# Kernel optimization log

Hardware: AMD Instinct MI355X
Metric: run time of the kernel (lower is better)

## Reference

```python
import jax, jax.numpy as jnp
import numpy as np
import math

WH, WW = 7, 7          # window size
N = WH * WW            # tokens per window = 49
H = 12                 # num heads
C = 384                # dim
D = C // H             # head dim = 32
NW = 64                # num windows (56x56 map, 7x7 windows)
B = 32                 # image batch
BW = B * NW            # windowed batch = 2048


def _cpb_constants():
    # log-spaced continuous relative coords table, flattened to [(2*WH-1)*(2*WW-1), 2]
    rh = np.arange(-(WH - 1), WH, dtype=np.float32)
    rw = np.arange(-(WW - 1), WW, dtype=np.float32)
    t = np.stack(np.meshgrid(rh, rw, indexing='ij'), axis=-1)  # [13,13,2]
    t[..., 0] /= (WH - 1)
    t[..., 1] /= (WW - 1)
    t *= 8.0
    t = np.sign(t) * np.log2(np.abs(t) + 1.0) / np.log2(8.0)
    # relative position index [N*N]
    ch, cw = np.meshgrid(np.arange(WH), np.arange(WW), indexing='ij')
    cf = np.stack([ch.ravel(), cw.ravel()])            # [2, N]
    rel = cf[:, :, None] - cf[:, None, :]              # [2, N, N]
    rel = rel.transpose(1, 2, 0).astype(np.int64)      # [N, N, 2]
    rel[..., 0] += WH - 1
    rel[..., 1] += WW - 1
    rel[..., 0] *= 2 * WW - 1
    rpi = rel.sum(-1).reshape(-1)                      # [N*N]
    return jnp.asarray(t.reshape(-1, 2)), jnp.asarray(rpi)

_COORDS_TABLE, _RPI = _cpb_constants()


def setup_inputs() -> dict:
    key = jax.random.key(0)
    ks = jax.random.split(key, 8)
    x = jax.random.normal(ks[0], (BW, N, C), dtype=jnp.float32)
    # shifted-window style 0/-100 mask
    mask = jnp.where(jax.random.uniform(ks[1], (NW, N, N)) < 0.1, -100.0, 0.0).astype(jnp.float32)
    qkv_w = jax.random.normal(ks[2], (3 * C, C), dtype=jnp.float32) * 0.02
    q_bias = jnp.zeros((C,), dtype=jnp.float32)
    v_bias = jnp.zeros((C,), dtype=jnp.float32)
    logit_scale = jnp.full((H, 1, 1), math.log(10.0), dtype=jnp.float32)
    cpb_w1 = jax.random.normal(ks[3], (512, 2), dtype=jnp.float32) * 0.02
    cpb_b1 = jnp.zeros((512,), dtype=jnp.float32)
    cpb_w2 = jax.random.normal(ks[4], (H, 512), dtype=jnp.float32) * 0.02
    proj_w = jax.random.normal(ks[5], (C, C), dtype=jnp.float32) * 0.02
    proj_b = jnp.zeros((C,), dtype=jnp.float32)
    return {"x": x, "mask": mask, "qkv_w": qkv_w, "q_bias": q_bias, "v_bias": v_bias,
            "logit_scale": logit_scale, "cpb_w1": cpb_w1, "cpb_b1": cpb_b1,
            "cpb_w2": cpb_w2, "proj_w": proj_w, "proj_b": proj_b}


def reference(x, mask, qkv_w, q_bias, v_bias, logit_scale, cpb_w1, cpb_b1, cpb_w2, proj_w, proj_b):
    B_, n, c = x.shape
    # qkv projection; k has no bias (registered zeros buffer)
    qkv_bias = jnp.concatenate([q_bias, jnp.zeros_like(q_bias), v_bias])
    qkv = x @ qkv_w.T + qkv_bias                              # [B_, N, 3C]
    qkv = qkv.reshape(B_, n, 3, H, D).transpose(2, 0, 3, 1, 4)  # [3, B_, H, N, D]
    q, k, v = qkv[0], qkv[1], qkv[2]
    # cosine attention
    qn = q / jnp.clip(jnp.linalg.norm(q, axis=-1, keepdims=True), 1e-12)
    kn = k / jnp.clip(jnp.linalg.norm(k, axis=-1, keepdims=True), 1e-12)
    attn = jnp.einsum('bhnd,bhmd->bhnm', qn, kn)              # [B_, H, N, N]
    scale = jnp.exp(jnp.minimum(logit_scale, math.log(1.0 / 0.01)))  # [H,1,1]
    attn = attn * scale
    # continuous position bias MLP + gather
    hid = jax.nn.relu(_COORDS_TABLE @ cpb_w1.T + cpb_b1)      # [169, 512]
    bias_tab = hid @ cpb_w2.T                                  # [169, H]
    rpb = bias_tab[_RPI].reshape(n, n, H).transpose(2, 0, 1)  # [H, N, N]
    rpb = 16.0 * jax.nn.sigmoid(rpb)
    attn = attn + rpb[None]
    # shifted-window mask add
    nW = mask.shape[0]
    attn = attn.reshape(B_ // nW, nW, H, n, n) + mask[None, :, None]
    attn = jax.nn.softmax(attn.reshape(B_, H, n, n), axis=-1)
    out = jnp.einsum('bhnm,bhmd->bnhd', attn, v).reshape(B_, n, c)
    return out @ proj_w.T + proj_b
```

## Files before the change

kernel.cpp:

```cpp
#include <hip/hip_runtime.h>
#include <hip/hip_bf16.h>
#include <math.h>

#define NTOK 49
#define NH 12
#define HD 32
#define CDIM 384
#define NWIN 64
#define BWIN 2048
#define QKVROW 1152

typedef __bf16 bf16x8 __attribute__((ext_vector_type(8)));
typedef __bf16 bf16x4 __attribute__((ext_vector_type(4)));
typedef float f32x4 __attribute__((ext_vector_type(4)));

__device__ __forceinline__ void gload_lds16(const void* g, void* l) {
    __builtin_amdgcn_global_load_lds((const __attribute__((address_space(1))) void*)g,
                                     (__attribute__((address_space(3))) void*)l, 16, 0, 0);
}

__global__ void cvt_f32_bf16(const float* __restrict__ src, __bf16* __restrict__ dst, int n8) {
    int i = blockIdx.x * blockDim.x + threadIdx.x;
    if (i >= n8) return;
    f32x4 a = *(const f32x4*)(src + (size_t)i * 8);
    f32x4 b = *(const f32x4*)(src + (size_t)i * 8 + 4);
    bf16x8 o;
#pragma unroll
    for (int e = 0; e < 4; ++e) { o[e] = (__bf16)a[e]; o[e + 4] = (__bf16)b[e]; }
    *(bf16x8*)(dst + (size_t)i * 8) = o;
}

__global__ void cpb_mlp_kernel(const float* __restrict__ w1, const float* __restrict__ b1,
                               const float* __restrict__ w2, float* __restrict__ bias_tab) {
    int t = blockIdx.x * blockDim.x + threadIdx.x;
    if (t >= 169 * NH) return;
    int r = t / NH, h = t - (t / NH) * NH;
    int i = r / 13, j = r - (r / 13) * 13;
    float a0 = (float)(i - 6) * (8.0f / 6.0f);
    float a1 = (float)(j - 6) * (8.0f / 6.0f);
    float c0 = copysignf(log2f(fabsf(a0) + 1.0f) * (1.0f / 3.0f), a0);
    float c1 = copysignf(log2f(fabsf(a1) + 1.0f) * (1.0f / 3.0f), a1);
    float sum = 0.f;
    for (int k = 0; k < 512; ++k) {
        float hid = c0 * w1[2 * k] + c1 * w1[2 * k + 1] + b1[k];
        hid = fmaxf(hid, 0.f);
        sum += hid * w2[h * 512 + k];
    }
    bias_tab[r * NH + h] = sum;
}

__global__ void rpbT_kernel(const float* __restrict__ bias_tab, float* __restrict__ rpbT) {
    int idx = blockIdx.x * blockDim.x + threadIdx.x;
    if (idx >= NH * NTOK * NTOK) return;
    int h = idx / (NTOK * NTOK);
    int rem = idx - h * (NTOK * NTOK);
    int kj = rem / NTOK, qi = rem - (rem / NTOK) * NTOK;
    int chi = qi / 7, cwi = qi - chi * 7;
    int chj = kj / 7, cwj = kj - chj * 7;
    int rpi = (chi - chj + 6) * 13 + (cwi - cwj + 6);
    float x = bias_tab[rpi * NH + h];
    rpbT[idx] = 16.f / (1.f + __expf(-x));
}

__global__ void maskT_kernel(const float* __restrict__ mask, float* __restrict__ maskT) {
    int idx = blockIdx.x * blockDim.x + threadIdx.x;
    if (idx >= NWIN * NTOK * NTOK) return;
    int w = idx / (NTOK * NTOK);
    int rem = idx - w * (NTOK * NTOK);
    int kj = rem / NTOK, qi = rem - (rem / NTOK) * NTOK;
    maskT[idx] = mask[(w * NTOK + qi) * NTOK + kj];
}

template <int MODE, int NBY>
__global__ __launch_bounds__(256) void gemm6(
    const __bf16* __restrict__ A, const __bf16* __restrict__ Bw,
    const float* __restrict__ qbias, const float* __restrict__ vbias,
    __bf16* __restrict__ qkvout,
    float* __restrict__ fout, const float* __restrict__ fbias)
{
    __shared__ __bf16 As[3][128 * 32];
    __shared__ __bf16 Bs[3][128 * 32];
    const int tid = threadIdx.x;
    const int chunk = (784 * NBY) >> 3;
    const int wg = (blockIdx.x & 7) * chunk + (blockIdx.x >> 3);
    const int gx = wg / NBY, gy = wg - (wg / NBY) * NBY;
    const int lane = tid & 63;
    const int wid = tid >> 6;
    const int wr = (wid >> 1) * 64;
    const int wc = (wid & 1) * 64;
    const int fr = lane & 15;
    const int fq = lane >> 4;

    f32x4 acc[4][4];
#pragma unroll
    for (int m = 0; m < 4; ++m)
#pragma unroll
        for (int n = 0; n < 4; ++n)
            acc[m][n] = (f32x4){0.f, 0.f, 0.f, 0.f};

    const int srow0 = tid >> 2, scp0 = tid & 3;
    const int srow1 = (256 + tid) >> 2;
    const size_t ar0 = (size_t)(gx * 128 + srow0) * CDIM + (scp0 ^ ((srow0 >> 1) & 3)) * 8;
    const size_t ar1 = (size_t)(gx * 128 + srow1) * CDIM + (scp0 ^ ((srow1 >> 1) & 3)) * 8;
    const size_t br0 = (size_t)(gy * 128 + srow0) * CDIM + (scp0 ^ ((srow0 >> 1) & 3)) * 8;
    const size_t br1 = (size_t)(gy * 128 + srow1) * CDIM + (scp0 ^ ((srow1 >> 1) & 3)) * 8;
    const int ls0 = tid * 16, ls1 = (256 + tid) * 16;

#define STAGE(ti, buf) do {                                              \
        const int kk_ = (ti) * 32;                                       \
        gload_lds16(A + ar0 + kk_, (char*)&As[buf][0] + ls0);            \
        gload_lds16(A + ar1 + kk_, (char*)&As[buf][0] + ls1);            \
        gload_lds16(Bw + br0 + kk_, (char*)&Bs[buf][0] + ls0);           \
        gload_lds16(Bw + br1 + kk_, (char*)&Bs[buf][0] + ls1);           \
    } while (0)

    STAGE(0, 0);
    STAGE(1, 1);

#pragma unroll
    for (int t = 0; t < 12; ++t) {
        if (t < 11) asm volatile("s_waitcnt vmcnt(4)" ::: "memory");
        else        asm volatile("s_waitcnt vmcnt(0)" ::: "memory");
        __builtin_amdgcn_s_barrier();
        if (t + 2 < 12) STAGE(t + 2, (t + 2) % 3);
        const int cur = t % 3;
        bf16x8 af[4], bfr[4];
#pragma unroll
        for (int m = 0; m < 4; ++m) {
            const int row = wr + m * 16 + fr;
            af[m] = *(const bf16x8*)&As[cur][row * 32 + (fq ^ ((row >> 1) & 3)) * 8];
        }
#pragma unroll
        for (int n = 0; n < 4; ++n) {
            const int row = wc + n * 16 + fr;
            bfr[n] = *(const bf16x8*)&Bs[cur][row * 32 + (fq ^ ((row >> 1) & 3)) * 8];
        }
#pragma unroll
        for (int m = 0; m < 4; ++m)
#pragma unroll
            for (int n = 0; n < 4; ++n)
                acc[m][n] = __builtin_amdgcn_mfma_f32_16x16x32_bf16(af[m], bfr[n], acc[m][n], 0, 0, 0);
    }
#undef STAGE

    if (MODE == 0) {
        const int colbase = gy * 128;
        const int part = colbase / CDIM;
        const int pcolbase = colbase - part * CDIM;
#pragma unroll
        for (int m = 0; m < 4; ++m) {
#pragma unroll
            for (int r = 0; r < 4; ++r) {
                const int row = gx * 128 + wr + m * 16 + fq * 4 + r;
                __bf16* orow = qkvout + (size_t)row * QKVROW + colbase + wc;
#pragma unroll
                for (int n = 0; n < 4; ++n) {
                    const int pcol = pcolbase + wc + n * 16 + fr;
                    float val = acc[m][n][r];
                    if (part == 0) val += qbias[pcol];
                    if (part == 2) val += vbias[pcol];
                    orow[n * 16 + fr] = (__bf16)val;
                }
            }
        }
    } else {
#pragma unroll
        for (int m = 0; m < 4; ++m) {
#pragma unroll
            for (int r = 0; r < 4; ++r) {
                const int row = gx * 128 + wr + m * 16 + fq * 4 + r;
                float* orow = fout + (size_t)row * CDIM + gy * 128 + wc;
#pragma unroll
                for (int n = 0; n < 4; ++n) {
                    const int col = gy * 128 + wc + n * 16 + fr;
                    orow[n * 16 + fr] = acc[m][n][r] + fbias[col];
                }
            }
        }
    }
}

#define WREG 15872
__global__ __launch_bounds__(256) void attn2(
    const __bf16* __restrict__ qkv, const float* __restrict__ maskT,
    const float* __restrict__ rpbT, const float* __restrict__ lscale,
    __bf16* __restrict__ aout)
{
    __shared__ char smem[4 * WREG];
    const int tid = threadIdx.x;
    const int wid = tid >> 6, lane = tid & 63;
    const int bh = blockIdx.x * 4 + wid;
    const int b = bh / NH, h = bh - b * NH;
    const int w = b & (NWIN - 1);
    const int c = lane & 15, g = lane >> 4;

    char* base = smem + wid * WREG;
    __bf16* Kl = (__bf16*)base;
    __bf16* Ql = (__bf16*)(base + 5120);
    __bf16* Vl = (__bf16*)(base + 10240);
    float* invq = (float*)(base + 15360);
    float* invk = (float*)(base + 15616);
    char* Pl = base;

    const float sc = __expf(fminf(lscale[h], 4.6051702f));

    {
        const int row = lane;
        const size_t rb = ((size_t)b * NTOK + row) * QKVROW + h * HD;
        bf16x8 z;
#pragma unroll
        for (int e = 0; e < 8; ++e) z[e] = (__bf16)0.f;
        {
            bf16x8 t[4];
            float ss = 0.f;
            if (row < NTOK) {
#pragma unroll
                for (int ch = 0; ch < 4; ++ch) {
                    t[ch] = *(const bf16x8*)(qkv + rb + ch * 8);
#pragma unroll
                    for (int e = 0; e < 8; ++e) { float f = (float)t[ch][e]; ss += f * f; }
                }
            } else {
#pragma unroll
                for (int ch = 0; ch < 4; ++ch) t[ch] = z;
            }
#pragma unroll
            for (int ch = 0; ch < 4; ++ch) *(bf16x8*)&Ql[row * 40 + ch * 8] = t[ch];
            invq[row] = sc / fmaxf(sqrtf(ss), 1e-12f);
        }
        {
            bf16x8 t[4];
            float ss = 0.f;
            if (row < NTOK) {
#pragma unroll
                for (int ch = 0; ch < 4; ++ch) {
                    t[ch] = *(const bf16x8*)(qkv + rb + CDIM + ch * 8);
#pragma unroll
                    for (int e = 0; e < 8; ++e) { float f = (float)t[ch][e]; ss += f * f; }
                }
            } else {
#pragma unroll
                for (int ch = 0; ch < 4; ++ch) t[ch] = z;
            }
#pragma unroll
            for (int ch = 0; ch < 4; ++ch) *(bf16x8*)&Kl[row * 40 + ch * 8] = t[ch];
            invk[row] = 1.f / fmaxf(sqrtf(ss), 1e-12f);
        }
        {
            bf16x8 t[4];
            if (row < NTOK) {
#pragma unroll
                for (int ch = 0; ch < 4; ++ch) t[ch] = *(const bf16x8*)(qkv + rb + 2 * CDIM + ch * 8);
            } else {
#pragma unroll
                for (int ch = 0; ch < 4; ++ch) t[ch] = z;
            }
#pragma unroll
            for (int ch = 0; ch < 4; ++ch) *(bf16x8*)&Vl[row * 40 + ch * 8] = t[ch];
        }
    }

    bf16x8 kfr[4], qfr[4];
#pragma unroll
    for (int mt = 0; mt < 4; ++mt) kfr[mt] = *(const bf16x8*)&Kl[(mt * 16 + c) * 40 + g * 8];
#pragma unroll
    for (int nt = 0; nt < 4; ++nt) qfr[nt] = *(const bf16x8*)&Ql[(nt * 16 + c) * 40 + g * 8];
    f32x4 S[4][4];
#pragma unroll
    for (int mt = 0; mt < 4; ++mt)
#pragma unroll
        for (int nt = 0; nt < 4; ++nt) {
            S[mt][nt] = (f32x4){0.f, 0.f, 0.f, 0.f};
            S[mt][nt] = __builtin_amdgcn_mfma_f32_16x16x32_bf16(kfr[mt], qfr[nt], S[mt][nt], 0, 0, 0);
        }

    const float* rp = rpbT + h * (NTOK * NTOK);
    const float* mk = maskT + w * (NTOK * NTOK);
    float ivq[4];
#pragma unroll
    for (int nt = 0; nt < 4; ++nt) ivq[nt] = invq[nt * 16 + c];
#pragma unroll
    for (int mt = 0; mt < 4; ++mt) {
#pragma unroll
        for (int r = 0; r < 4; ++r) {
            const int k = mt * 16 + g * 4 + r;
            const float ivk = invk[k];
#pragma unroll
            for (int nt = 0; nt < 4; ++nt) {
                const int q = nt * 16 + c;
                float v = S[mt][nt][r] * ivk * ivq[nt];
                if (k < NTOK) {
                    if (q < NTOK) v += rp[k * NTOK + q] + mk[k * NTOK + q];
                } else {
                    v = -1e30f;
                }
                S[mt][nt][r] = v;
            }
        }
    }

    float rs[4];
#pragma unroll
    for (int nt = 0; nt < 4; ++nt) {
        float m = -1e30f;
#pragma unroll
        for (int mt = 0; mt < 4; ++mt)
#pragma unroll
            for (int r = 0; r < 4; ++r) m = fmaxf(m, S[mt][nt][r]);
        m = fmaxf(m, __shfl_xor(m, 16));
        m = fmaxf(m, __shfl_xor(m, 32));
        float s = 0.f;
#pragma unroll
        for (int mt = 0; mt < 4; ++mt)
#pragma unroll
            for (int r = 0; r < 4; ++r) {
                float e = __expf(S[mt][nt][r] - m);
                S[mt][nt][r] = e;
                s += e;
            }
        s += __shfl_xor(s, 16);
        s += __shfl_xor(s, 32);
        rs[nt] = 1.f / s;
    }

#pragma unroll
    for (int mt = 0; mt < 4; ++mt)
#pragma unroll
        for (int nt = 0; nt < 4; ++nt) {
            bf16x4 pk;
#pragma unroll
            for (int r = 0; r < 4; ++r) pk[r] = (__bf16)(S[mt][nt][r] * rs[nt]);
            *(bf16x4*)(Pl + (nt * 16 + c) * 144 + (mt * 16 + g * 4) * 2) = pk;
        }

    bf16x8 vfr[2][2];
#pragma unroll
    for (int kt = 0; kt < 2; ++kt)
#pragma unroll
        for (int dt = 0; dt < 2; ++dt) {
            bf16x8 t;
#pragma unroll
            for (int e = 0; e < 8; ++e) t[e] = Vl[(kt * 32 + g * 8 + e) * 40 + dt * 16 + c];
            vfr[kt][dt] = t;
        }
    f32x4 O[4][2];
#pragma unroll
    for (int mt = 0; mt < 4; ++mt)
#pragma unroll
        for (int dt = 0; dt < 2; ++dt) O[mt][dt] = (f32x4){0.f, 0.f, 0.f, 0.f};
#pragma unroll
    for (int mt = 0; mt < 4; ++mt)
#pragma unroll
        for (int kt = 0; kt < 2; ++kt) {
            bf16x8 pfr = *(const bf16x8*)(Pl + (mt * 16 + c) * 144 + kt * 64 + g * 16);
#pragma unroll
            for (int dt = 0; dt < 2; ++dt)
                O[mt][dt] = __builtin_amdgcn_mfma_f32_16x16x32_bf16(pfr, vfr[kt][dt], O[mt][dt], 0, 0, 0);
        }

#pragma unroll
    for (int mt = 0; mt < 4; ++mt)
#pragma unroll
        for (int r = 0; r < 4; ++r) {
            const int q = mt * 16 + g * 4 + r;
            if (q < NTOK) {
                const size_t off = ((size_t)b * NTOK + q) * CDIM + h * HD;
                aout[off + c] = (__bf16)O[mt][0][r];
                aout[off + 16 + c] = (__bf16)O[mt][1][r];
            }
        }
}

extern "C" void kernel_launch(void* const* d_in, const int* in_sizes, int n_in,
                              void* d_out, int out_size, void* d_ws, size_t ws_size,
                              hipStream_t stream) {
    const float* x      = (const float*)d_in[0];
    const float* mask   = (const float*)d_in[1];
    const float* qkv_w  = (const float*)d_in[2];
    const float* q_bias = (const float*)d_in[3];
    const float* v_bias = (const float*)d_in[4];
    const float* lscale = (const float*)d_in[5];
    const float* cpb_w1 = (const float*)d_in[6];
    const float* cpb_b1 = (const float*)d_in[7];
    const float* cpb_w2 = (const float*)d_in[8];
    const float* proj_w = (const float*)d_in[9];
    const float* proj_b = (const float*)d_in[10];
    float* out = (float*)d_out;

    const size_t NROWS = (size_t)BWIN * NTOK;
    __bf16* qkvbuf  = (__bf16*)d_ws;
    __bf16* xbf     = qkvbuf + NROWS * QKVROW;
    __bf16* aoutbuf = xbf;
    __bf16* qkv_wb  = xbf + NROWS * CDIM;
    __bf16* proj_wb = qkv_wb + QKVROW * CDIM;
    float*  bias_tab = (float*)(proj_wb + CDIM * CDIM);
    float*  rpbT   = bias_tab + 169 * NH;
    float*  maskT  = rpbT + NH * NTOK * NTOK;

    hipLaunchKernelGGL(cvt_f32_bf16, dim3((int)((NROWS * CDIM / 8 + 255) / 256)), dim3(256), 0, stream,
                       x, xbf, (int)(NROWS * CDIM / 8));
    hipLaunchKernelGGL(cvt_f32_bf16, dim3((QKVROW * CDIM / 8 + 255) / 256), dim3(256), 0, stream,
                       qkv_w, qkv_wb, QKVROW * CDIM / 8);
    hipLaunchKernelGGL(cvt_f32_bf16, dim3((CDIM * CDIM / 8 + 255) / 256), dim3(256), 0, stream,
                       proj_w, proj_wb, CDIM * CDIM / 8);
    hipLaunchKernelGGL(cpb_mlp_kernel, dim3(8), dim3(256), 0, stream,
                       cpb_w1, cpb_b1, cpb_w2, bias_tab);
    hipLaunchKernelGGL(rpbT_kernel, dim3((NH * NTOK * NTOK + 255) / 256), dim3(256), 0, stream,
                       bias_tab, rpbT);
    hipLaunchKernelGGL(maskT_kernel, dim3((NWIN * NTOK * NTOK + 255) / 256), dim3(256), 0, stream,
                       mask, maskT);
    hipLaunchKernelGGL((gemm6<0, 9>), dim3(784 * 9), dim3(256), 0, stream,
                       xbf, qkv_wb, q_bias, v_bias, qkvbuf, (float*)nullptr,
                       (const float*)nullptr);
    hipLaunchKernelGGL(attn2, dim3(BWIN * NH / 4), dim3(256), 0, stream,
                       qkvbuf, maskT, rpbT, lscale, aoutbuf);
    hipLaunchKernelGGL((gemm6<1, 3>), dim3(784 * 3), dim3(256), 0, stream,
                       aoutbuf, proj_wb, (const float*)nullptr, (const float*)nullptr,
                       (__bf16*)nullptr, out, proj_b);
}
```

Baseline: 451.8 us.

## Fuse x fp32-to-bf16 conversion into QKV GEMM and coalesce attention loads

The QKV GEMM now loads fp32 x tiles directly into LDS through global_load_lds and converts them to bf16 when reading fragments. This removes the separate conversion kernel and its full write and re-read of a bf16 copy of x. The cost is double the LDS footprint for the A tile and extra global reads of fp32 data inside the GEMM, and the GEMM is re-run for each of the 9 column tiles. The attention kernel now gives each block 4 consecutive heads of one window and loads Q/K/V cooperatively into LDS with coalesced 16-byte loads, then computes the norms from LDS after a barrier.

```diff
diff --git a/kernel.cpp b/kernel.cpp
--- a/kernel.cpp
+++ b/kernel.cpp
@@ -71,19 +71,125 @@
     maskT[idx] = mask[(w * NTOK + qi) * NTOK + kj];
 }
 
-template <int MODE, int NBY>
-__global__ __launch_bounds__(256) void gemm6(
+__global__ __launch_bounds__(256) void gemm_qkv2(
+    const float* __restrict__ X, const __bf16* __restrict__ Bw,
+    const float* __restrict__ qbias, const float* __restrict__ vbias,
+    __bf16* __restrict__ qkvout)
+{
+    __shared__ float Asf[3][128 * 32];
+    __shared__ __bf16 Bs[3][128 * 32];
+    const int tid = threadIdx.x;
+    const int chunkg = (784 * 9) >> 3;
+    const int wg = (blockIdx.x & 7) * chunkg + (blockIdx.x >> 3);
+    const int gx = wg / 9, gy = wg - (wg / 9) * 9;
+    const int lane = tid & 63;
+    const int wid = tid >> 6;
+    const int wr = (wid >> 1) * 64;
+    const int wc = (wid & 1) * 64;
+    const int fr = lane & 15;
+    const int fq = lane >> 4;
+
+    f32x4 acc[4][4];
+#pragma unroll
+    for (int m = 0; m < 4; ++m)
+#pragma unroll
+        for (int n = 0; n < 4; ++n)
+            acc[m][n] = (f32x4){0.f, 0.f, 0.f, 0.f};
+
+    size_t asrc[4];
+    int adst[4];
+#pragma unroll
+    for (int i = 0; i < 4; ++i) {
+        const int s = i * 256 + tid;
+        const int row = s >> 3, cp = s & 7;
+        asrc[i] = (size_t)(gx * 128 + row) * CDIM + (cp ^ (row & 7)) * 4;
+        adst[i] = s * 16;
+    }
+    size_t bsrc[2];
+    int bdst[2];
+#pragma unroll
+    for (int j = 0; j < 2; ++j) {
+        const int s = j * 256 + tid;
+        const int row = s >> 2, cp = s & 3;
+        bsrc[j] = (size_t)(gy * 128 + row) * CDIM + (cp ^ ((row >> 1) & 3)) * 8;
+        bdst[j] = s * 16;
+    }
+
+#define STAGEQ(ti, buf) do {                                              \
+        const int kk_ = (ti) * 32;                                        \
+        gload_lds16(X + asrc[0] + kk_, (char*)&Asf[buf][0] + adst[0]);    \
+        gload_lds16(X + asrc[1] + kk_, (char*)&Asf[buf][0] + adst[1]);    \
+        gload_lds16(X + asrc[2] + kk_, (char*)&Asf[buf][0] + adst[2]);    \
+        gload_lds16(X + asrc[3] + kk_, (char*)&Asf[buf][0] + adst[3]);    \
+        gload_lds16(Bw + bsrc[0] + kk_, (char*)&Bs[buf][0] + bdst[0]);    \
+        gload_lds16(Bw + bsrc[1] + kk_, (char*)&Bs[buf][0] + bdst[1]);    \
+    } while (0)
+
+    STAGEQ(0, 0);
+    STAGEQ(1, 1);
+
+#pragma unroll
+    for (int t = 0; t < 12; ++t) {
+        if (t < 11) asm volatile("s_waitcnt vmcnt(6)" ::: "memory");
+        else        asm volatile("s_waitcnt vmcnt(0)" ::: "memory");
+        __builtin_amdgcn_s_barrier();
+        if (t + 2 < 12) STAGEQ(t + 2, (t + 2) % 3);
+        const int cur = t % 3;
+        bf16x8 af[4], bfr[4];
+#pragma unroll
+        for (int m = 0; m < 4; ++m) {
+            const int row = wr + m * 16 + fr;
+            f32x4 lo = *(const f32x4*)&Asf[cur][row * 32 + ((2 * fq) ^ (row & 7)) * 4];
+            f32x4 hi = *(const f32x4*)&Asf[cur][row * 32 + ((2 * fq + 1) ^ (row & 7)) * 4];
+            bf16x8 v;
+#pragma unroll
+            for (int e = 0; e < 4; ++e) { v[e] = (__bf16)lo[e]; v[e + 4] = (__bf16)hi[e]; }
+            af[m] = v;
+        }
+#pragma unroll
+        for (int n = 0; n < 4; ++n) {
+            const int row = wc + n * 16 + fr;
+            bfr[n] = *(const bf16x8*)&Bs[cur][row * 32 + (fq ^ ((row >> 1) & 3)) * 8];
+        }
+#pragma unroll
+        for (int m = 0; m < 4; ++m)
+#pragma unroll
+            for (int n = 0; n < 4; ++n)
+                acc[m][n] = __builtin_amdgcn_mfma_f32_16x16x32_bf16(af[m], bfr[n], acc[m][n], 0, 0, 0);
+    }
+#undef STAGEQ
+
+    const int colbase = gy * 128;
+    const int part = colbase / CDIM;
+    const int pcolbase = colbase - part * CDIM;
+#pragma unroll
+    for (int m = 0; m < 4; ++m) {
+#pragma unroll
+        for (int r = 0; r < 4; ++r) {
+            const int row = gx * 128 + wr + m * 16 + fq * 4 + r;
+            __bf16* orow = qkvout + (size_t)row * QKVROW + colbase + wc;
+#pragma unroll
+            for (int n = 0; n < 4; ++n) {
+                const int pcol = pcolbase + wc + n * 16 + fr;
+                float val = acc[m][n][r];
+                if (part == 0) val += qbias[pcol];
+                if (part == 2) val += vbias[pcol];
+                orow[n * 16 + fr] = (__bf16)val;
+            }
+        }
+    }
+}
+
+__global__ __launch_bounds__(256) void gemm_proj(
     const __bf16* __restrict__ A, const __bf16* __restrict__ Bw,
-    const float* __restrict__ qbias, const float* __restrict__ vbias,
-    __bf16* __restrict__ qkvout,
     float* __restrict__ fout, const float* __restrict__ fbias)
 {
     __shared__ __bf16 As[3][128 * 32];
     __shared__ __bf16 Bs[3][128 * 32];
     const int tid = threadIdx.x;
-    const int chunk = (784 * NBY) >> 3;
+    const int chunk = (784 * 3) >> 3;
     const int wg = (blockIdx.x & 7) * chunk + (blockIdx.x >> 3);
-    const int gx = wg / NBY, gy = wg - (wg / NBY) * NBY;
+    const int gx = wg / 3, gy = wg - (wg / 3) * 3;
     const int lane = tid & 63;
     const int wid = tid >> 6;
     const int wr = (wid >> 1) * 64;
@@ -143,45 +249,23 @@
     }
 #undef STAGE
 
-    if (MODE == 0) {
-        const int colbase = gy * 128;
-        const int part = colbase / CDIM;
-        const int pcolbase = colbase - part * CDIM;
-#pragma unroll
-        for (int m = 0; m < 4; ++m) {
-#pragma unroll
-            for (int r = 0; r < 4; ++r) {
-                const int row = gx * 128 + wr + m * 16 + fq * 4 + r;
-                __bf16* orow = qkvout + (size_t)row * QKVROW + colbase + wc;
-#pragma unroll
-                for (int n = 0; n < 4; ++n) {
-                    const int pcol = pcolbase + wc + n * 16 + fr;
-                    float val = acc[m][n][r];
-                    if (part == 0) val += qbias[pcol];
-                    if (part == 2) val += vbias[pcol];
-                    orow[n * 16 + fr] = (__bf16)val;
-                }
-            }
-        }
-    } else {
-#pragma unroll
-        for (int m = 0; m < 4; ++m) {
-#pragma unroll
-            for (int r = 0; r < 4; ++r) {
-                const int row = gx * 128 + wr + m * 16 + fq * 4 + r;
-                float* orow = fout + (size_t)row * CDIM + gy * 128 + wc;
-#pragma unroll
-                for (int n = 0; n < 4; ++n) {
-                    const int col = gy * 128 + wc + n * 16 + fr;
-                    orow[n * 16 + fr] = acc[m][n][r] + fbias[col];
-                }
+#pragma unroll
+    for (int m = 0; m < 4; ++m) {
+#pragma unroll
+        for (int r = 0; r < 4; ++r) {
+            const int row = gx * 128 + wr + m * 16 + fq * 4 + r;
+            float* orow = fout + (size_t)row * CDIM + gy * 128 + wc;
+#pragma unroll
+            for (int n = 0; n < 4; ++n) {
+                const int col = gy * 128 + wc + n * 16 + fr;
+                orow[n * 16 + fr] = acc[m][n][r] + fbias[col];
             }
         }
     }
 }
 
 #define WREG 15872
-__global__ __launch_bounds__(256) void attn2(
+__global__ __launch_bounds__(256) void attn3(
     const __bf16* __restrict__ qkv, const float* __restrict__ maskT,
     const float* __restrict__ rpbT, const float* __restrict__ lscale,
     __bf16* __restrict__ aout)
@@ -189,10 +273,34 @@
     __shared__ char smem[4 * WREG];
     const int tid = threadIdx.x;
     const int wid = tid >> 6, lane = tid & 63;
-    const int bh = blockIdx.x * 4 + wid;
-    const int b = bh / NH, h = bh - b * NH;
+    const int blk = blockIdx.x;
+    const int b = blk / 3;
+    const int h0 = (blk - b * 3) * 4;
+    const int h = h0 + wid;
     const int w = b & (NWIN - 1);
     const int c = lane & 15, g = lane >> 4;
+
+    {
+        bf16x8 z;
+#pragma unroll
+        for (int e = 0; e < 8; ++e) z[e] = (__bf16)0.f;
+        const int matoff[3] = {5120, 0, 10240};
+#pragma unroll
+        for (int p = 0; p < 3; ++p) {
+#pragma unroll
+            for (int i = 0; i < 4; ++i) {
+                const int s = i * 256 + tid;
+                const int row = s >> 4, chunk = s & 15;
+                const int head = chunk >> 2, hch = chunk & 3;
+                bf16x8 v = z;
+                if (row < NTOK)
+                    v = *(const bf16x8*)(qkv + ((size_t)b * NTOK + row) * QKVROW
+                                         + p * CDIM + h0 * HD + chunk * 8);
+                *(bf16x8*)(smem + head * WREG + matoff[p] + row * 80 + hch * 16) = v;
+            }
+        }
+    }
+    __syncthreads();
 
     char* base = smem + wid * WREG;
     __bf16* Kl = (__bf16*)base;
@@ -206,58 +314,22 @@
 
     {
         const int row = lane;
-        const size_t rb = ((size_t)b * NTOK + row) * QKVROW + h * HD;
-        bf16x8 z;
-#pragma unroll
-        for (int e = 0; e < 8; ++e) z[e] = (__bf16)0.f;
-        {
-            bf16x8 t[4];
-            float ss = 0.f;
-            if (row < NTOK) {
-#pragma unroll
-                for (int ch = 0; ch < 4; ++ch) {
-                    t[ch] = *(const bf16x8*)(qkv + rb + ch * 8);
-#pragma unroll
-                    for (int e = 0; e < 8; ++e) { float f = (float)t[ch][e]; ss += f * f; }
-                }
-            } else {
-#pragma unroll
-                for (int ch = 0; ch < 4; ++ch) t[ch] = z;
-            }
-#pragma unroll
-            for (int ch = 0; ch < 4; ++ch) *(bf16x8*)&Ql[row * 40 + ch * 8] = t[ch];
-            invq[row] = sc / fmaxf(sqrtf(ss), 1e-12f);
-        }
-        {
-            bf16x8 t[4];
-            float ss = 0.f;
-            if (row < NTOK) {
-#pragma unroll
-                for (int ch = 0; ch < 4; ++ch) {
-                    t[ch] = *(const bf16x8*)(qkv + rb + CDIM + ch * 8);
-#pragma unroll
-                    for (int e = 0; e < 8; ++e) { float f = (float)t[ch][e]; ss += f * f; }
-                }
-            } else {
-#pragma unroll
-                for (int ch = 0; ch < 4; ++ch) t[ch] = z;
-            }
-#pragma unroll
-            for (int ch = 0; ch < 4; ++ch) *(bf16x8*)&Kl[row * 40 + ch * 8] = t[ch];
-            invk[row] = 1.f / fmaxf(sqrtf(ss), 1e-12f);
-        }
-        {
-            bf16x8 t[4];
-            if (row < NTOK) {
-#pragma unroll
-                for (int ch = 0; ch < 4; ++ch) t[ch] = *(const bf16x8*)(qkv + rb + 2 * CDIM + ch * 8);
-            } else {
-#pragma unroll
-                for (int ch = 0; ch < 4; ++ch) t[ch] = z;
-            }
-#pragma unroll
-            for (int ch = 0; ch < 4; ++ch) *(bf16x8*)&Vl[row * 40 + ch * 8] = t[ch];
-        }
+        float ss = 0.f;
+#pragma unroll
+        for (int ch = 0; ch < 4; ++ch) {
+            bf16x8 tq = *(const bf16x8*)&Ql[row * 40 + ch * 8];
+#pragma unroll
+            for (int e = 0; e < 8; ++e) { float f = (float)tq[e]; ss += f * f; }
+        }
+        invq[row] = sc / fmaxf(sqrtf(ss), 1e-12f);
+        ss = 0.f;
+#pragma unroll
+        for (int ch = 0; ch < 4; ++ch) {
+            bf16x8 tk = *(const bf16x8*)&Kl[row * 40 + ch * 8];
+#pragma unroll
+            for (int e = 0; e < 8; ++e) { float f = (float)tk[e]; ss += f * f; }
+        }
+        invk[row] = 1.f / fmaxf(sqrtf(ss), 1e-12f);
     }
 
     bf16x8 kfr[4], qfr[4];
@@ -389,16 +461,13 @@
 
     const size_t NROWS = (size_t)BWIN * NTOK;
     __bf16* qkvbuf  = (__bf16*)d_ws;
-    __bf16* xbf     = qkvbuf + NROWS * QKVROW;
-    __bf16* aoutbuf = xbf;
-    __bf16* qkv_wb  = xbf + NROWS * CDIM;
+    __bf16* aoutbuf = qkvbuf + NROWS * QKVROW;
+    __bf16* qkv_wb  = aoutbuf + NROWS * CDIM;
     __bf16* proj_wb = qkv_wb + QKVROW * CDIM;
     float*  bias_tab = (float*)(proj_wb + CDIM * CDIM);
     float*  rpbT   = bias_tab + 169 * NH;
     float*  maskT  = rpbT + NH * NTOK * NTOK;
 
-    hipLaunchKernelGGL(cvt_f32_bf16, dim3((int)((NROWS * CDIM / 8 + 255) / 256)), dim3(256), 0, stream,
-                       x, xbf, (int)(NROWS * CDIM / 8));
     hipLaunchKernelGGL(cvt_f32_bf16, dim3((QKVROW * CDIM / 8 + 255) / 256), dim3(256), 0, stream,
                        qkv_w, qkv_wb, QKVROW * CDIM / 8);
     hipLaunchKernelGGL(cvt_f32_bf16, dim3((CDIM * CDIM / 8 + 255) / 256), dim3(256), 0, stream,
@@ -409,12 +478,10 @@
                        bias_tab, rpbT);
     hipLaunchKernelGGL(maskT_kernel, dim3((NWIN * NTOK * NTOK + 255) / 256), dim3(256), 0, stream,
                        mask, maskT);
-    hipLaunchKernelGGL((gemm6<0, 9>), dim3(784 * 9), dim3(256), 0, stream,
-                       xbf, qkv_wb, q_bias, v_bias, qkvbuf, (float*)nullptr,
-                       (const float*)nullptr);
-    hipLaunchKernelGGL(attn2, dim3(BWIN * NH / 4), dim3(256), 0, stream,
+    hipLaunchKernelGGL(gemm_qkv2, dim3(784 * 9), dim3(256), 0, stream,
+                       x, qkv_wb, q_bias, v_bias, qkvbuf);
+    hipLaunchKernelGGL(attn3, dim3(BWIN * 3), dim3(256), 0, stream,
                        qkvbuf, maskT, rpbT, lscale, aoutbuf);
-    hipLaunchKernelGGL((gemm6<1, 3>), dim3(784 * 3), dim3(256), 0, stream,
-                       aoutbuf, proj_wb, (const float*)nullptr, (const float*)nullptr,
-                       (__bf16*)nullptr, out, proj_b);
-}
+    hipLaunchKernelGGL(gemm_proj, dim3(784 * 3), dim3(256), 0, stream,
+                       aoutbuf, proj_wb, out, proj_b);
+}
```

After: 598.1 us. 1.32x slower.
